# Kernel tuning notes

Hardware: AMD Instinct MI355X
Metric: run time of the kernel (lower is better)

Reference implementation:

```python
import jax, jax.numpy as jnp
import numpy as np

B, C1, C2, CF, H, W, NH = 1, 64, 256, 256, 64, 64, 8
HD = CF // NH
EPS = 1e-5


def setup_inputs() -> dict:
    key = jax.random.key(0)
    ks = jax.random.split(key, 12)
    s = 0.02
    return {
        "F_lidar": jax.random.normal(ks[0], (B, C1, H, W), jnp.float32),
        "F_cam": jax.random.normal(ks[1], (B, C2, H, W), jnp.float32),
        "Wq": jax.random.normal(ks[2], (CF, C1), jnp.float32) * s,
        "Wk": jax.random.normal(ks[3], (CF, C2), jnp.float32) * s,
        "Wv": jax.random.normal(ks[4], (CF, C2), jnp.float32) * s,
        "Wo": jax.random.normal(ks[5], (CF, CF), jnp.float32) * s,
        "Wres": jax.random.normal(ks[6], (CF, C1), jnp.float32) * s,
        "ln1_g": jnp.ones((CF,), jnp.float32),
        "ln1_b": jnp.zeros((CF,), jnp.float32),
        "ln2_g": jnp.ones((CF,), jnp.float32),
        "ln2_b": jnp.zeros((CF,), jnp.float32),
        "W1": jax.random.normal(ks[7], (4 * CF, CF), jnp.float32) * s,
        "b1": jnp.zeros((4 * CF,), jnp.float32),
        "W2": jax.random.normal(ks[8], (CF, 4 * CF), jnp.float32) * s,
        "b2": jnp.zeros((CF,), jnp.float32),
    }


def _ln(x, g, b):
    m = jnp.mean(x, axis=-1, keepdims=True)
    v = jnp.mean((x - m) ** 2, axis=-1, keepdims=True)
    return (x - m) * jax.lax.rsqrt(v + EPS) * g + b


def reference(F_lidar, F_cam, Wq, Wk, Wv, Wo, Wres, ln1_g, ln1_b, ln2_g, ln2_b, W1, b1, W2, b2):
    N = H * W
    # 1x1 convs == per-token linear projections on flattened tokens
    tok_l = F_lidar.reshape(B, C1, N).transpose(0, 2, 1)  # (B, N, C1)
    tok_c = F_cam.reshape(B, C2, N).transpose(0, 2, 1)    # (B, N, C2)
    Q = (tok_l @ Wq.T).reshape(B, N, NH, HD)
    K = (tok_c @ Wk.T).reshape(B, N, NH, HD)
    V = (tok_c @ Wv.T).reshape(B, N, NH, HD)
    scale = HD ** -0.5
    scores = jnp.einsum("bnhd,bmhd->bhnm", Q, K) * scale  # (B, NH, N, N)
    attn = jax.nn.softmax(scores, axis=-1)
    out = jnp.einsum("bhnm,bmhd->bnhd", attn, V).reshape(B, N, CF)
    out = out @ Wo.T                                      # out_proj (1x1 conv)
    res = tok_l @ Wres.T                                  # residual_proj
    x = _ln(res + out, ln1_g, ln1_b)
    # FFN (dropout is identity in eval)
    h = jax.nn.relu(x @ W1.T + b1)
    ffn = h @ W2.T + b2
    x = _ln(x + ffn, ln2_g, ln2_b)
    return x.transpose(0, 2, 1).reshape(B, CF, H, W)
```

## Files before the change

kernel.cpp:

```cpp
#include <hip/hip_runtime.h>
#include <math.h>

#define NTOK 4096
#define C1 64
#define C2 256
#define CF 256
#define NH 8
#define HD 32
#define CFF 1024
#define EPSF 1e-5f
#define SPLIT 4
#define KVBLK 128
#define QSCALE 0.25505654040876564f

using f32x4  = __attribute__((ext_vector_type(4))) float;
using bf16x8 = __attribute__((ext_vector_type(8))) short;
using u32x4  = __attribute__((ext_vector_type(4))) unsigned int;
typedef unsigned short ushort_t;

__device__ inline ushort_t f2bf(float x) {
    union { float f; unsigned int u; } v; v.f = x;
    unsigned int r = (v.u + 0x7FFFu + ((v.u >> 16) & 1u)) >> 16;
    return (ushort_t)r;
}
__device__ inline float bf2f(ushort_t u) {
    union { unsigned int i; float f; } v; v.i = ((unsigned int)u) << 16; return v.f;
}
__device__ inline unsigned int fbits(float x) {
    union { float f; unsigned int u; } v; v.f = x; return v.u;
}

__device__ inline float exp2_raw(float x) {
#if __has_builtin(__builtin_amdgcn_exp2f)
    return __builtin_amdgcn_exp2f(x);
#else
    float r;
    asm("v_exp_f32 %0, %1" : "=v"(r) : "v"(x));
    return r;
#endif
}

__global__ __launch_bounds__(256) void prep_kernel(
    const float* __restrict__ Wq, const float* __restrict__ Wk,
    const float* __restrict__ Wv, const float* __restrict__ Wo,
    const float* __restrict__ Wres, const float* __restrict__ W1,
    const float* __restrict__ W2, const float* __restrict__ F_lidar,
    const float* __restrict__ F_cam,
    ushort_t* oWq, ushort_t* oWk, ushort_t* oWv, ushort_t* oWo,
    ushort_t* oWres, ushort_t* oW1, ushort_t* oW2,
    ushort_t* __restrict__ Flt, ushort_t* __restrict__ Fct) {
    __shared__ float tls[32][33];
    int b = blockIdx.x;
    if (b < 736) {
        const float* src; ushort_t* dst; int base, lgK; bool tiled;
        if      (b < 16)  { src = Wq;   dst = oWq;   base = b;       lgK = 6;  tiled = false; }
        else if (b < 80)  { src = Wk;   dst = oWk;   base = b - 16;  lgK = 8;  tiled = false; }
        else if (b < 144) { src = Wv;   dst = oWv;   base = b - 80;  lgK = 8;  tiled = false; }
        else if (b < 208) { src = Wo;   dst = oWo;   base = b - 144; lgK = 8;  tiled = true; }
        else if (b < 224) { src = Wres; dst = oWres; base = b - 208; lgK = 6;  tiled = true; }
        else if (b < 480) { src = W1;   dst = oW1;   base = b - 224; lgK = 8;  tiled = true; }
        else              { src = W2;   dst = oW2;   base = b - 480; lgK = 10; tiled = true; }
        const int i = base * 1024 + threadIdx.x * 4;
        const float4 v = *(const float4*)(src + i);
        ushort4 pk;
        pk.x = f2bf(v.x); pk.y = f2bf(v.y); pk.z = f2bf(v.z); pk.w = f2bf(v.w);
        if (!tiled) {
            *(ushort4*)(dst + i) = pk;
        } else {
            const int c  = i >> lgK;
            const int kk = i & ((1 << lgK) - 1);
            const int tau = (c >> 8) * (1 << (lgK - 6)) + (kk >> 6);
            const int dst4 = tau * 16384 + (c & 255) * 64
                           + (((((kk >> 3) & 7)) ^ (c & 7)) << 3) + (kk & 7);
            *(ushort4*)(dst + dst4) = pk;
        }
        return;
    }
    b -= 736;
    const float* src; ushort_t* dst; int C, c0, n0;
    if (b < 256) { src = F_lidar; dst = Flt; C = C1; c0 = (b & 1) * 32; n0 = (b >> 1) * 32; }
    else { b -= 256; src = F_cam; dst = Fct; C = C2; c0 = (b & 7) * 32; n0 = (b >> 3) * 32; }
    const int tx = threadIdx.x & 31, ty = threadIdx.x >> 5;
#pragma unroll
    for (int i = 0; i < 32; i += 8) tls[ty + i][tx] = src[(size_t)(c0 + ty + i) * NTOK + n0 + tx];
    __syncthreads();
#pragma unroll
    for (int i = 0; i < 32; i += 8) dst[(size_t)(n0 + ty + i) * C + c0 + tx] = f2bf(tls[tx][ty + i]);
}

__global__ __launch_bounds__(256) void qkv_kernel(
    const ushort_t* __restrict__ Flt, const ushort_t* __restrict__ Fct,
    const ushort_t* __restrict__ Wqb, const ushort_t* __restrict__ Wkb,
    const ushort_t* __restrict__ Wvb,
    ushort_t* __restrict__ Qb, ushort_t* __restrict__ Kb, ushort_t* __restrict__ Vt) {
    const int z = blockIdx.z;
    const ushort_t* A = (z == 0) ? Flt : Fct;
    const ushort_t* W = (z == 0) ? Wqb : (z == 1) ? Wkb : Wvb;
    const int K = (z == 0) ? C1 : C2;

    const int tid = threadIdx.x;
    const int wid = tid >> 6, lane = tid & 63;
    const int g = lane >> 4, r = lane & 15;
    const int r0 = blockIdx.x * 128 + wid * 16;
    const int c0 = blockIdx.y * 64;

    f32x4 acc[2][4];
#pragma unroll
    for (int i = 0; i < 2; ++i)
#pragma unroll
        for (int t = 0; t < 4; ++t) acc[i][t] = (f32x4){0, 0, 0, 0};

    const ushort_t* ap0 = A + (size_t)(r0 + r) * K + (g << 3);
    const ushort_t* ap1 = ap0 + (size_t)64 * K;
    const ushort_t* wp = W + (size_t)(c0 + r) * K + (g << 3);
#pragma unroll 2
    for (int k0 = 0; k0 < K; k0 += 32) {
        const bf16x8 a0 = *(const bf16x8*)(ap0 + k0);
        const bf16x8 a1 = *(const bf16x8*)(ap1 + k0);
#pragma unroll
        for (int t = 0; t < 4; ++t) {
            const bf16x8 wf = *(const bf16x8*)(wp + (size_t)(t * 16) * K + k0);
            acc[0][t] = __builtin_amdgcn_mfma_f32_16x16x32_bf16(a0, wf, acc[0][t], 0, 0, 0);
            acc[1][t] = __builtin_amdgcn_mfma_f32_16x16x32_bf16(a1, wf, acc[1][t], 0, 0, 0);
        }
    }
    if (z == 0) {
#pragma unroll
        for (int i = 0; i < 2; ++i)
#pragma unroll
            for (int t = 0; t < 4; ++t) {
                const int col = c0 + 16 * t + r;
#pragma unroll
                for (int q = 0; q < 4; ++q)
                    Qb[(size_t)(r0 + i * 64 + 4 * g + q) * CF + col] = f2bf(acc[i][t][q] * QSCALE);
            }
    } else if (z == 1) {
#pragma unroll
        for (int i = 0; i < 2; ++i)
#pragma unroll
            for (int t = 0; t < 4; ++t) {
                const int col = c0 + 16 * t + r;
#pragma unroll
                for (int q = 0; q < 4; ++q) {
                    const int tok = r0 + i * 64 + 4 * g + q;
                    const int cs = (col & ~31) | ((((col >> 3) & 3) ^ ((tok >> 1) & 3)) << 3) | (col & 7);
                    Kb[(size_t)tok * CF + cs] = f2bf(acc[i][t][q]);
                }
            }
    } else {
#pragma unroll
        for (int i = 0; i < 2; ++i)
#pragma unroll
            for (int t = 0; t < 4; ++t) {
                const int dglob = c0 + 16 * t + r;
                const int hh = dglob >> 5, d = dglob & 31;
                const int tok0 = r0 + i * 64 + 4 * g;
                const int T = tok0 >> 7, tl = tok0 & 127;
                const int kc = tl >> 5, gp = (tl >> 2) & 3, jh = (tl >> 4) & 1;
                const int c = kc * 4 + gp;
                ushort4 pk;
                pk.x = f2bf(acc[i][t][0]); pk.y = f2bf(acc[i][t][1]);
                pk.z = f2bf(acc[i][t][2]); pk.w = f2bf(acc[i][t][3]);
                *(ushort4*)((char*)Vt + ((size_t)(hh * 32 + T) << 13)
                            + ((size_t)(c * 32 + (d ^ (c & 7))) << 4) + (jh << 3)) = pk;
            }
    }
}

__global__ __launch_bounds__(512, 4) void fattn_kernel(const ushort_t* __restrict__ Qb,
                                                       const ushort_t* __restrict__ Kb,
                                                       const ushort_t* __restrict__ Vt,
                                                       ushort_t* __restrict__ Opart,
                                                       float* __restrict__ Lst) {
    __shared__ ushort_t Ks[3][4096];
    __shared__ ushort_t Vs[2][4096];

    const int tid = threadIdx.x;
    const int wid = tid >> 6, lane = tid & 63;
    const int g = lane >> 4, r = lane & 15;
    const int bid = blockIdx.x;
    const int qb = bid & 15;
    const int sp = (bid >> 4) & (SPLIT - 1);
    const int h  = bid >> 6;
    const int n0 = qb * 256 + wid * 32;
    const int m_beg = sp * (NTOK / SPLIT);

    const bf16x8 qfA = *(const bf16x8*)(Qb + ((size_t)(n0 + r) << 8) + h * HD + (g << 3));
    const bf16x8 qfB = *(const bf16x8*)(Qb + ((size_t)(n0 + 16 + r) << 8) + h * HD + (g << 3));
    const bf16x8 onesf = {(short)0x3F80, (short)0x3F80, (short)0x3F80, (short)0x3F80,
                          (short)0x3F80, (short)0x3F80, (short)0x3F80, (short)0x3F80};

    const char* kb  = (const char*)Ks[0] + (r << 6) + ((g ^ ((r >> 1) & 3)) << 4);
    const char* vbg = (const char*)Vs[0] + (g << 9) + ((r & 8) << 4);
    const int slotbase = ((r & 7) ^ g) << 4;

    const int o = tid << 4;
    const char* ksrc = (const char*)Kb + (size_t)(m_beg + (o >> 6)) * 512 + (h << 6) + (o & 63);
    const char* vsrc = (const char*)Vt + ((size_t)(h * 32 + (m_beg >> 7)) << 13) + o;

    auto stageK = [&](int buf) {
        __builtin_amdgcn_global_load_lds(
            (const __attribute__((address_space(1))) unsigned int*)ksrc,
            (__attribute__((address_space(3))) unsigned int*)((char*)Ks[buf] + (wid << 10)), 16, 0, 0);
        ksrc += KVBLK * 512;
    };
    auto stageV = [&](int buf) {
        __builtin_amdgcn_global_load_lds(
            (const __attribute__((address_space(1))) unsigned int*)vsrc,
            (__attribute__((address_space(3))) unsigned int*)((char*)Vs[buf] + (wid << 10)), 16, 0, 0);
        vsrc += 8192;
    };

    f32x4 accA0 = {0, 0, 0, 0}, accA1 = {0, 0, 0, 0}, laccA = {0, 0, 0, 0};
    f32x4 accB0 = {0, 0, 0, 0}, accB1 = {0, 0, 0, 0}, laccB = {0, 0, 0, 0};

    stageK(0);
    stageV(0);
    stageK(1);
    asm volatile("s_waitcnt vmcnt(1)" ::: "memory");
    __builtin_amdgcn_s_barrier();

    constexpr int NT = (NTOK / SPLIT) / KVBLK;
#pragma unroll
    for (int tt = 0; tt < NT; ++tt) {
        if (tt + 1 < NT) stageV((tt + 1) & 1);
        if (tt + 2 < NT) stageK((tt + 2) % 3);
        const int kofs = (tt % 3) << 13;
        const int vofs = (tt & 1) << 13;

        f32x4 sA[8], sB[8];
#pragma unroll
        for (int t8 = 0; t8 < 8; ++t8) {
            const bf16x8 kf = *(const bf16x8*)(kb + kofs + (t8 << 10));
            sA[t8] = __builtin_amdgcn_mfma_f32_16x16x32_bf16(kf, qfA, (f32x4){0, 0, 0, 0}, 0, 0, 0);
            sB[t8] = __builtin_amdgcn_mfma_f32_16x16x32_bf16(kf, qfB, (f32x4){0, 0, 0, 0}, 0, 0, 0);
        }
        u32x4 pkvA[4], pkvB[4];
#pragma unroll
        for (int t8 = 0; t8 < 8; ++t8) {
            const float a0 = exp2_raw(sA[t8][0]);
            const float a1 = exp2_raw(sA[t8][1]);
            const float a2 = exp2_raw(sA[t8][2]);
            const float a3 = exp2_raw(sA[t8][3]);
            pkvA[t8 >> 1][(t8 & 1) * 2]     = __builtin_amdgcn_perm(fbits(a1), fbits(a0), 0x07060302u);
            pkvA[t8 >> 1][(t8 & 1) * 2 + 1] = __builtin_amdgcn_perm(fbits(a3), fbits(a2), 0x07060302u);
        }
#pragma unroll
        for (int t8 = 0; t8 < 8; ++t8) {
            const float b0 = exp2_raw(sB[t8][0]);
            const float b1 = exp2_raw(sB[t8][1]);
            const float b2 = exp2_raw(sB[t8][2]);
            const float b3 = exp2_raw(sB[t8][3]);
            pkvB[t8 >> 1][(t8 & 1) * 2]     = __builtin_amdgcn_perm(fbits(b1), fbits(b0), 0x07060302u);
            pkvB[t8 >> 1][(t8 & 1) * 2 + 1] = __builtin_amdgcn_perm(fbits(b3), fbits(b2), 0x07060302u);
        }
#pragma unroll
        for (int kc = 0; kc < 4; ++kc) {
            union { u32x4 u; bf16x8 b; } puA, puB;
            puA.u = pkvA[kc]; puB.u = pkvB[kc];
            const bf16x8 pfA = puA.b, pfB = puB.b;
            laccA = __builtin_amdgcn_mfma_f32_16x16x32_bf16(pfA, onesf, laccA, 0, 0, 0);
            laccB = __builtin_amdgcn_mfma_f32_16x16x32_bf16(pfB, onesf, laccB, 0, 0, 0);
            const char* va = vbg + vofs + (kc << 11) + (slotbase ^ ((kc & 1) << 6));
            const bf16x8 vf0 = *(const bf16x8*)(va);
            const bf16x8 vf1 = *(const bf16x8*)(va + 256);
            accA0 = __builtin_amdgcn_mfma_f32_16x16x32_bf16(pfA, vf0, accA0, 0, 0, 0);
            accB0 = __builtin_amdgcn_mfma_f32_16x16x32_bf16(pfB, vf0, accB0, 0, 0, 0);
            accA1 = __builtin_amdgcn_mfma_f32_16x16x32_bf16(pfA, vf1, accA1, 0, 0, 0);
            accB1 = __builtin_amdgcn_mfma_f32_16x16x32_bf16(pfB, vf1, accB1, 0, 0, 0);
        }
        if (tt + 2 < NT)      { asm volatile("s_waitcnt vmcnt(1)" ::: "memory"); }
        else                  { asm volatile("s_waitcnt vmcnt(0)" ::: "memory"); }
        __builtin_amdgcn_s_barrier();
    }
    const size_t baseA = (size_t)(sp * NH + h) * NTOK + n0;
    const size_t baseB = baseA + 16;
    if (r == 0) {
        *(f32x4*)(Lst + baseA + 4 * g) = laccA;
        *(f32x4*)(Lst + baseB + 4 * g) = laccB;
    }
#pragma unroll
    for (int q = 0; q < 4; ++q) {
        const size_t rowbA = (baseA + 4 * g + q) * HD;
        Opart[rowbA + r]      = f2bf(accA0[q]);
        Opart[rowbA + 16 + r] = f2bf(accA1[q]);
        const size_t rowbB = (baseB + 4 * g + q) * HD;
        Opart[rowbB + r]      = f2bf(accB0[q]);
        Opart[rowbB + 16 + r] = f2bf(accB1[q]);
    }
}

__global__ __launch_bounds__(512) void tail_kernel(
    const ushort_t* __restrict__ Opart, const float* __restrict__ Lst,
    const ushort_t* __restrict__ Wo,
    const ushort_t* __restrict__ Flt, const ushort_t* __restrict__ Wres,
    const float* __restrict__ g1, const float* __restrict__ bt1,
    const ushort_t* __restrict__ W1, const float* __restrict__ b1,
    const ushort_t* __restrict__ W2, const float* __restrict__ b2,
    const float* __restrict__ g2, const float* __restrict__ bt2,
    float* __restrict__ out) {
    __shared__ ushort_t Wb[3][16384];
    __shared__ ushort_t As[16][264];
    __shared__ ushort_t Xs[16][264];
    __shared__ ushort_t Hs[16][1032];
    __shared__ ushort_t Fs[16][72];
    __shared__ float Bias[2304];
    __shared__ float redS[8][16], redQ[8][16];
    const int tid = threadIdx.x;
    const int wid = tid >> 6, lane = tid & 63;
    const int g = lane >> 4, r = lane & 15;
    const int row0 = blockIdx.x * 16;
    const int cw = wid * 32;

    const int wl00 = (cw + r) * 128 + ((g ^ (r & 7)) << 4);
    const int wl01 = wl00 + 2048;
    const int wl10 = (cw + r) * 128 + (((4 + g) ^ (r & 7)) << 4);
    const int wl11 = wl10 + 2048;

    const int wslice = (wid << 12) + ((lane & 63) << 4);
    auto stageW = [&](const ushort_t* src, int buf) {
        const char* s = (const char*)src + wslice;
        char* d = (char*)&Wb[buf][0] + wslice;
#pragma unroll
        for (int j = 0; j < 4; ++j) {
            __builtin_amdgcn_global_load_lds(
                (const __attribute__((address_space(1))) unsigned int*)(s + j * 1024),
                (__attribute__((address_space(3))) unsigned int*)(d + j * 1024), 16, 0, 0);
        }
    };
    auto wsrc = [&](int s) -> const ushort_t* {
        if (s < 4)  return Wo + (size_t)s * 16384;
        if (s == 4) return Wres;
        if (s < 21) return W1 + (size_t)(s - 5) * 16384;
        return W2 + (size_t)(s - 21) * 16384;
    };

    {
        const int ri = tid >> 5;
        const int cc = (tid & 31) << 3;
        const int h  = cc >> 5, d0 = cc & 31;
        const int n  = row0 + ri;
        float L = 0.f;
#pragma unroll
        for (int s = 0; s < SPLIT; ++s) L += Lst[(size_t)(s * NH + h) * NTOK + n];
        const float invL = 1.f / L;
        float o[8] = {0.f, 0.f, 0.f, 0.f, 0.f, 0.f, 0.f, 0.f};
#pragma unroll
        for (int s = 0; s < SPLIT; ++s) {
            const ushort_t* p = Opart + ((size_t)(s * NH + h) * NTOK + n) * HD + d0;
            const ushort4 a = *(const ushort4*)p;
            const ushort4 b = *(const ushort4*)(p + 4);
            o[0] += bf2f(a.x); o[1] += bf2f(a.y); o[2] += bf2f(a.z); o[3] += bf2f(a.w);
            o[4] += bf2f(b.x); o[5] += bf2f(b.y); o[6] += bf2f(b.z); o[7] += bf2f(b.w);
        }
        ushort4 m0, m1;
        m0.x = f2bf(o[0] * invL); m0.y = f2bf(o[1] * invL);
        m0.z = f2bf(o[2] * invL); m0.w = f2bf(o[3] * invL);
        m1.x = f2bf(o[4] * invL); m1.y = f2bf(o[5] * invL);
        m1.z = f2bf(o[6] * invL); m1.w = f2bf(o[7] * invL);
        *(ushort4*)&As[ri][cc]     = m0;
        *(ushort4*)&As[ri][cc + 4] = m1;
        *(ushort2*)&Fs[ri][(tid & 31) * 2] =
            *(const ushort2*)(Flt + (size_t)(row0 + ri) * C1 + (tid & 31) * 2);
#pragma unroll
        for (int i5 = 0; i5 < 5; ++i5) {
            const int i = i5 * 512 + tid;
            if (i < 2304) {
                float v;
                if      (i < 256)  v = g1[i];
                else if (i < 512)  v = bt1[i - 256];
                else if (i < 768)  v = b2[i - 512];
                else if (i < 1024) v = g2[i - 768];
                else if (i < 1280) v = bt2[i - 1024];
                else               v = b1[i - 1280];
                Bias[i] = v;
            }
        }
    }
    __syncthreads();

    stageW(wsrc(0), 0);
    stageW(wsrc(1), 1);

    f32x4 accB[2] = {{0, 0, 0, 0}, {0, 0, 0, 0}};
#pragma unroll
    for (int t = 0; t < 5; ++t) {
        stageW(wsrc(t + 2), (t + 2) % 3);
        asm volatile("s_waitcnt vmcnt(8)" ::: "memory");
        const char* wb = (const char*)&Wb[t % 3][0];
        const bf16x8 w00 = *(const bf16x8*)(wb + wl00);
        const bf16x8 w01 = *(const bf16x8*)(wb + wl01);
        const bf16x8 w10 = *(const bf16x8*)(wb + wl10);
        const bf16x8 w11 = *(const bf16x8*)(wb + wl11);
        bf16x8 af0, af1;
        if (t < 4) {
            af0 = *(const bf16x8*)&As[r][t * 64 + (g << 3)];
            af1 = *(const bf16x8*)&As[r][t * 64 + 32 + (g << 3)];
        } else {
            af0 = *(const bf16x8*)&Fs[r][(g << 3)];
            af1 = *(const bf16x8*)&Fs[r][32 + (g << 3)];
        }
        accB[0] = __builtin_amdgcn_mfma_f32_16x16x32_bf16(af0, w00, accB[0], 0, 0, 0);
        accB[1] = __builtin_amdgcn_mfma_f32_16x16x32_bf16(af0, w01, accB[1], 0, 0, 0);
        accB[0] = __builtin_amdgcn_mfma_f32_16x16x32_bf16(af1, w10, accB[0], 0, 0, 0);
        accB[1] = __builtin_amdgcn_mfma_f32_16x16x32_bf16(af1, w11, accB[1], 0, 0, 0);
    }
    f32x4 xv[2];
    {
        f32x4 sv, qv;
#pragma unroll
        for (int q = 0; q < 4; ++q) {
            float s = accB[0][q] + accB[1][q];
            float sq = fmaf(accB[0][q], accB[0][q], accB[1][q] * accB[1][q]);
            s += __shfl_xor(s, 1); s += __shfl_xor(s, 2); s += __shfl_xor(s, 4); s += __shfl_xor(s, 8);
            sq += __shfl_xor(sq, 1); sq += __shfl_xor(sq, 2); sq += __shfl_xor(sq, 4); sq += __shfl_xor(sq, 8);
            sv[q] = s; qv[q] = sq;
        }
        if (r == 0) { *(f32x4*)&redS[wid][4 * g] = sv; *(f32x4*)&redQ[wid][4 * g] = qv; }
        __syncthreads();
        f32x4 S = {0, 0, 0, 0}, SQ = {0, 0, 0, 0};
#pragma unroll
        for (int w = 0; w < 8; ++w) {
            S  += *(const f32x4*)&redS[w][4 * g];
            SQ += *(const f32x4*)&redQ[w][4 * g];
        }
        f32x4 mn4, rs4;
#pragma unroll
        for (int q = 0; q < 4; ++q) {
            mn4[q] = S[q] * (1.f / CF);
            rs4[q] = rsqrtf(fmaxf(SQ[q] * (1.f / CF) - mn4[q] * mn4[q], 0.f) + EPSF);
        }
#pragma unroll
        for (int t = 0; t < 2; ++t) {
            const int col = cw + 16 * t + r;
            const float gam = Bias[col], bet = Bias[256 + col];
#pragma unroll
            for (int q = 0; q < 4; ++q) {
                xv[t][q] = (accB[t][q] - mn4[q]) * rs4[q] * gam + bet;
                Xs[4 * g + q][col] = f2bf(xv[t][q]);
            }
        }
    }
    __syncthreads();

    {
        f32x4 acc1[8];
#pragma unroll
        for (int t = 0; t < 8; ++t) acc1[t] = (f32x4){0, 0, 0, 0};
#pragma unroll
        for (int t = 5; t < 21; ++t) {
            stageW(wsrc(t + 2), (t + 2) % 3);
            asm volatile("s_waitcnt vmcnt(8)" ::: "memory");
            const int tc = t - 5;
            const char* wb = (const char*)&Wb[t % 3][0];
            const bf16x8 w00 = *(const bf16x8*)(wb + wl00);
            const bf16x8 w01 = *(const bf16x8*)(wb + wl01);
            const bf16x8 w10 = *(const bf16x8*)(wb + wl10);
            const bf16x8 w11 = *(const bf16x8*)(wb + wl11);
            const bf16x8 af0 = *(const bf16x8*)&Xs[r][(tc & 3) * 64 + (g << 3)];
            const bf16x8 af1 = *(const bf16x8*)&Xs[r][(tc & 3) * 64 + 32 + (g << 3)];
            const int idx = (tc >> 2) * 2;
            acc1[idx]     = __builtin_amdgcn_mfma_f32_16x16x32_bf16(w00, af0, acc1[idx], 0, 0, 0);
            acc1[idx + 1] = __builtin_amdgcn_mfma_f32_16x16x32_bf16(w01, af0, acc1[idx + 1], 0, 0, 0);
            acc1[idx]     = __builtin_amdgcn_mfma_f32_16x16x32_bf16(w10, af1, acc1[idx], 0, 0, 0);
            acc1[idx + 1] = __builtin_amdgcn_mfma_f32_16x16x32_bf16(w11, af1, acc1[idx + 1], 0, 0, 0);
        }
#pragma unroll
        for (int idx = 0; idx < 8; ++idx) {
            const int colb = (idx >> 1) * 256 + cw + 16 * (idx & 1) + 4 * g;
            const f32x4 bv = *(const f32x4*)&Bias[1280 + colb];
            ushort4 hw;
            hw.x = f2bf(fmaxf(acc1[idx][0] + bv[0], 0.f));
            hw.y = f2bf(fmaxf(acc1[idx][1] + bv[1], 0.f));
            hw.z = f2bf(fmaxf(acc1[idx][2] + bv[2], 0.f));
            hw.w = f2bf(fmaxf(acc1[idx][3] + bv[3], 0.f));
            *(ushort4*)&Hs[r][colb] = hw;
        }
    }
    __syncthreads();

    f32x4 accD[2] = {{0, 0, 0, 0}, {0, 0, 0, 0}};
#pragma unroll
    for (int t = 21; t < 37; ++t) {
        if (t + 2 < 37) {
            stageW(wsrc(t + 2), (t + 2) % 3);
            asm volatile("s_waitcnt vmcnt(8)" ::: "memory");
        } else if (t + 1 < 37) {
            asm volatile("s_waitcnt vmcnt(4)" ::: "memory");
        } else {
            asm volatile("s_waitcnt vmcnt(0)" ::: "memory");
        }
        const int tc = t - 21;
        const char* wb = (const char*)&Wb[t % 3][0];
        const bf16x8 w00 = *(const bf16x8*)(wb + wl00);
        const bf16x8 w01 = *(const bf16x8*)(wb + wl01);
        const bf16x8 w10 = *(const bf16x8*)(wb + wl10);
        const bf16x8 w11 = *(const bf16x8*)(wb + wl11);
        const bf16x8 af0 = *(const bf16x8*)&Hs[r][tc * 64 + (g << 3)];
        const bf16x8 af1 = *(const bf16x8*)&Hs[r][tc * 64 + 32 + (g << 3)];
        accD[0] = __builtin_amdgcn_mfma_f32_16x16x32_bf16(af0, w00, accD[0], 0, 0, 0);
        accD[1] = __builtin_amdgcn_mfma_f32_16x16x32_bf16(af0, w01, accD[1], 0, 0, 0);
        accD[0] = __builtin_amdgcn_mfma_f32_16x16x32_bf16(af1, w10, accD[0], 0, 0, 0);
        accD[1] = __builtin_amdgcn_mfma_f32_16x16x32_bf16(af1, w11, accD[1], 0, 0, 0);
    }
    {
#pragma unroll
        for (int t = 0; t < 2; ++t) {
            const float bb = Bias[512 + cw + 16 * t + r];
#pragma unroll
            for (int q = 0; q < 4; ++q) accD[t][q] += bb + xv[t][q];
        }
        f32x4 sv, qv;
#pragma unroll
        for (int q = 0; q < 4; ++q) {
            float s = accD[0][q] + accD[1][q];
            float sq = fmaf(accD[0][q], accD[0][q], accD[1][q] * accD[1][q]);
            s += __shfl_xor(s, 1); s += __shfl_xor(s, 2); s += __shfl_xor(s, 4); s += __shfl_xor(s, 8);
            sq += __shfl_xor(sq, 1); sq += __shfl_xor(sq, 2); sq += __shfl_xor(sq, 4); sq += __shfl_xor(sq, 8);
            sv[q] = s; qv[q] = sq;
        }
        __syncthreads();
        if (r == 0) { *(f32x4*)&redS[wid][4 * g] = sv; *(f32x4*)&redQ[wid][4 * g] = qv; }
        __syncthreads();
        f32x4 S = {0, 0, 0, 0}, SQ = {0, 0, 0, 0};
#pragma unroll
        for (int w = 0; w < 8; ++w) {
            S  += *(const f32x4*)&redS[w][4 * g];
            SQ += *(const f32x4*)&redQ[w][4 * g];
        }
        f32x4 mn4, rs4;
#pragma unroll
        for (int q = 0; q < 4; ++q) {
            mn4[q] = S[q] * (1.f / CF);
            rs4[q] = rsqrtf(fmaxf(SQ[q] * (1.f / CF) - mn4[q] * mn4[q], 0.f) + EPSF);
        }
#pragma unroll
        for (int t = 0; t < 2; ++t) {
            const int col = cw + 16 * t + r;
            const float gam = Bias[768 + col], bet = Bias[1024 + col];
            f32x4 ov;
#pragma unroll
            for (int q = 0; q < 4; ++q)
                ov[q] = (accD[t][q] - mn4[q]) * rs4[q] * gam + bet;
            *(f32x4*)(out + (size_t)col * NTOK + row0 + 4 * g) = ov;
        }
    }
}

extern "C" void kernel_launch(void* const* d_in, const int* in_sizes, int n_in,
                              void* d_out, int out_size, void* d_ws, size_t ws_size,
                              hipStream_t stream) {
    const float* F_lidar = (const float*)d_in[0];
    const float* F_cam   = (const float*)d_in[1];
    const float* Wq      = (const float*)d_in[2];
    const float* Wk      = (const float*)d_in[3];
    const float* Wv      = (const float*)d_in[4];
    const float* Wo      = (const float*)d_in[5];
    const float* Wres    = (const float*)d_in[6];
    const float* ln1_g   = (const float*)d_in[7];
    const float* ln1_b   = (const float*)d_in[8];
    const float* ln2_g   = (const float*)d_in[9];
    const float* ln2_b   = (const float*)d_in[10];
    const float* W1      = (const float*)d_in[11];
    const float* b1      = (const float*)d_in[12];
    const float* W2      = (const float*)d_in[13];
    const float* b2      = (const float*)d_in[14];
    float* out = (float*)d_out;
    char* ws = (char*)d_ws;

    const size_t KB = 1024, MB = 1024 * 1024;
    ushort_t* Wq_b   = (ushort_t*)(ws + 0);
    ushort_t* Wk_b   = (ushort_t*)(ws + 32 * KB);
    ushort_t* Wv_b   = (ushort_t*)(ws + 160 * KB);
    ushort_t* Wo_b   = (ushort_t*)(ws + 288 * KB);
    ushort_t* Wres_b = (ushort_t*)(ws + 416 * KB);
    ushort_t* W1_b   = (ushort_t*)(ws + 448 * KB);
    ushort_t* W2_b   = (ushort_t*)(ws + 960 * KB);
    ushort_t* Flt    = (ushort_t*)(ws + 1536 * KB);
    ushort_t* Fct    = (ushort_t*)(ws + 2 * MB);
    ushort_t* Qb     = (ushort_t*)(ws + 4 * MB);
    ushort_t* Kb     = (ushort_t*)(ws + 6 * MB);
    ushort_t* Vt     = (ushort_t*)(ws + 8 * MB);
    ushort_t* Opart  = (ushort_t*)(ws + 12 * MB);
    float*    Lst    = (float*)(ws + 20 * MB);

    prep_kernel<<<2016, 256, 0, stream>>>(Wq, Wk, Wv, Wo, Wres, W1, W2, F_lidar, F_cam,
                                          Wq_b, Wk_b, Wv_b, Wo_b, Wres_b, W1_b, W2_b, Flt, Fct);
    qkv_kernel<<<dim3(NTOK / 128, CF / 64, 3), 256, 0, stream>>>(Flt, Fct, Wq_b, Wk_b, Wv_b, Qb, Kb, Vt);
    fattn_kernel<<<NH * SPLIT * (NTOK / 256), 512, 0, stream>>>(Qb, Kb, Vt, Opart, Lst);
    tail_kernel<<<NTOK / 16, 512, 0, stream>>>(Opart, Lst, Wo_b, Flt, Wres_b, ln1_g, ln1_b,
                                               W1_b, b1, W2_b, b2, ln2_g, ln2_b, out);
}
```

Measured before the change: 63.62 us.

## Double per-wave query rows in flash attention to reuse K/V tiles

Each wave in the attention kernel now processes 64 query rows instead of 32 (four 16-row fragments), and each block covers 512 queries, so the grid is halved. K fragments are loaded into registers once and reused across four QK MFMAs, and each V fragment feeds four PV MFMAs. This halves K/V staging traffic and LDS reads per query. The cost is much higher register pressure (launch bounds lowered from 4 to 2 blocks per CU) and only 256 blocks, which may underfill the GPU and reduce latency hiding.

```diff
diff --git a/kernel.cpp b/kernel.cpp
--- a/kernel.cpp
+++ b/kernel.cpp
@@ -167,7 +167,7 @@
     }
 }
 
-__global__ __launch_bounds__(512, 4) void fattn_kernel(const ushort_t* __restrict__ Qb,
+__global__ __launch_bounds__(512, 2) void fattn_kernel(const ushort_t* __restrict__ Qb,
                                                        const ushort_t* __restrict__ Kb,
                                                        const ushort_t* __restrict__ Vt,
                                                        ushort_t* __restrict__ Opart,
@@ -179,14 +179,16 @@
     const int wid = tid >> 6, lane = tid & 63;
     const int g = lane >> 4, r = lane & 15;
     const int bid = blockIdx.x;
-    const int qb = bid & 15;
-    const int sp = (bid >> 4) & (SPLIT - 1);
-    const int h  = bid >> 6;
-    const int n0 = qb * 256 + wid * 32;
+    const int qb = bid & 7;
+    const int sp = (bid >> 3) & (SPLIT - 1);
+    const int h  = bid >> 5;
+    const int n0 = qb * 512 + wid * 64;
     const int m_beg = sp * (NTOK / SPLIT);
 
-    const bf16x8 qfA = *(const bf16x8*)(Qb + ((size_t)(n0 + r) << 8) + h * HD + (g << 3));
-    const bf16x8 qfB = *(const bf16x8*)(Qb + ((size_t)(n0 + 16 + r) << 8) + h * HD + (g << 3));
+    bf16x8 qf[4];
+#pragma unroll
+    for (int i = 0; i < 4; ++i)
+        qf[i] = *(const bf16x8*)(Qb + ((size_t)(n0 + 16 * i + r) << 8) + h * HD + (g << 3));
     const bf16x8 onesf = {(short)0x3F80, (short)0x3F80, (short)0x3F80, (short)0x3F80,
                           (short)0x3F80, (short)0x3F80, (short)0x3F80, (short)0x3F80};
 
@@ -211,8 +213,13 @@
         vsrc += 8192;
     };
 
-    f32x4 accA0 = {0, 0, 0, 0}, accA1 = {0, 0, 0, 0}, laccA = {0, 0, 0, 0};
-    f32x4 accB0 = {0, 0, 0, 0}, accB1 = {0, 0, 0, 0}, laccB = {0, 0, 0, 0};
+    f32x4 acc0[4], acc1[4], lacc[4];
+#pragma unroll
+    for (int i = 0; i < 4; ++i) {
+        acc0[i] = (f32x4){0, 0, 0, 0};
+        acc1[i] = (f32x4){0, 0, 0, 0};
+        lacc[i] = (f32x4){0, 0, 0, 0};
+    }
 
     stageK(0);
     stageV(0);
@@ -228,65 +235,86 @@
         const int kofs = (tt % 3) << 13;
         const int vofs = (tt & 1) << 13;
 
-        f32x4 sA[8], sB[8];
-#pragma unroll
-        for (int t8 = 0; t8 < 8; ++t8) {
-            const bf16x8 kf = *(const bf16x8*)(kb + kofs + (t8 << 10));
-            sA[t8] = __builtin_amdgcn_mfma_f32_16x16x32_bf16(kf, qfA, (f32x4){0, 0, 0, 0}, 0, 0, 0);
-            sB[t8] = __builtin_amdgcn_mfma_f32_16x16x32_bf16(kf, qfB, (f32x4){0, 0, 0, 0}, 0, 0, 0);
-        }
-        u32x4 pkvA[4], pkvB[4];
-#pragma unroll
-        for (int t8 = 0; t8 < 8; ++t8) {
-            const float a0 = exp2_raw(sA[t8][0]);
-            const float a1 = exp2_raw(sA[t8][1]);
-            const float a2 = exp2_raw(sA[t8][2]);
-            const float a3 = exp2_raw(sA[t8][3]);
-            pkvA[t8 >> 1][(t8 & 1) * 2]     = __builtin_amdgcn_perm(fbits(a1), fbits(a0), 0x07060302u);
-            pkvA[t8 >> 1][(t8 & 1) * 2 + 1] = __builtin_amdgcn_perm(fbits(a3), fbits(a2), 0x07060302u);
-        }
-#pragma unroll
-        for (int t8 = 0; t8 < 8; ++t8) {
-            const float b0 = exp2_raw(sB[t8][0]);
-            const float b1 = exp2_raw(sB[t8][1]);
-            const float b2 = exp2_raw(sB[t8][2]);
-            const float b3 = exp2_raw(sB[t8][3]);
-            pkvB[t8 >> 1][(t8 & 1) * 2]     = __builtin_amdgcn_perm(fbits(b1), fbits(b0), 0x07060302u);
-            pkvB[t8 >> 1][(t8 & 1) * 2 + 1] = __builtin_amdgcn_perm(fbits(b3), fbits(b2), 0x07060302u);
+        bf16x8 kfr[8];
+#pragma unroll
+        for (int t8 = 0; t8 < 8; ++t8)
+            kfr[t8] = *(const bf16x8*)(kb + kofs + (t8 << 10));
+
+        u32x4 pkv[4][4];
+        {
+            f32x4 sA[8], sB[8];
+#pragma unroll
+            for (int t8 = 0; t8 < 8; ++t8) {
+                sA[t8] = __builtin_amdgcn_mfma_f32_16x16x32_bf16(kfr[t8], qf[0], (f32x4){0, 0, 0, 0}, 0, 0, 0);
+                sB[t8] = __builtin_amdgcn_mfma_f32_16x16x32_bf16(kfr[t8], qf[1], (f32x4){0, 0, 0, 0}, 0, 0, 0);
+            }
+#pragma unroll
+            for (int t8 = 0; t8 < 8; ++t8) {
+                const float a0 = exp2_raw(sA[t8][0]);
+                const float a1 = exp2_raw(sA[t8][1]);
+                const float a2 = exp2_raw(sA[t8][2]);
+                const float a3 = exp2_raw(sA[t8][3]);
+                pkv[0][t8 >> 1][(t8 & 1) * 2]     = __builtin_amdgcn_perm(fbits(a1), fbits(a0), 0x07060302u);
+                pkv[0][t8 >> 1][(t8 & 1) * 2 + 1] = __builtin_amdgcn_perm(fbits(a3), fbits(a2), 0x07060302u);
+                const float b0 = exp2_raw(sB[t8][0]);
+                const float b1 = exp2_raw(sB[t8][1]);
+                const float b2 = exp2_raw(sB[t8][2]);
+                const float b3 = exp2_raw(sB[t8][3]);
+                pkv[1][t8 >> 1][(t8 & 1) * 2]     = __builtin_amdgcn_perm(fbits(b1), fbits(b0), 0x07060302u);
+                pkv[1][t8 >> 1][(t8 & 1) * 2 + 1] = __builtin_amdgcn_perm(fbits(b3), fbits(b2), 0x07060302u);
+            }
+        }
+        {
+            f32x4 sA[8], sB[8];
+#pragma unroll
+            for (int t8 = 0; t8 < 8; ++t8) {
+                sA[t8] = __builtin_amdgcn_mfma_f32_16x16x32_bf16(kfr[t8], qf[2], (f32x4){0, 0, 0, 0}, 0, 0, 0);
+                sB[t8] = __builtin_amdgcn_mfma_f32_16x16x32_bf16(kfr[t8], qf[3], (f32x4){0, 0, 0, 0}, 0, 0, 0);
+            }
+#pragma unroll
+            for (int t8 = 0; t8 < 8; ++t8) {
+                const float a0 = exp2_raw(sA[t8][0]);
+                const float a1 = exp2_raw(sA[t8][1]);
+                const float a2 = exp2_raw(sA[t8][2]);
+                const float a3 = exp2_raw(sA[t8][3]);
+                pkv[2][t8 >> 1][(t8 & 1) * 2]     = __builtin_amdgcn_perm(fbits(a1), fbits(a0), 0x07060302u);
+                pkv[2][t8 >> 1][(t8 & 1) * 2 + 1] = __builtin_amdgcn_perm(fbits(a3), fbits(a2), 0x07060302u);
+                const float b0 = exp2_raw(sB[t8][0]);
+                const float b1 = exp2_raw(sB[t8][1]);
+                const float b2 = exp2_raw(sB[t8][2]);
+                const float b3 = exp2_raw(sB[t8][3]);
+                pkv[3][t8 >> 1][(t8 & 1) * 2]     = __builtin_amdgcn_perm(fbits(b1), fbits(b0), 0x07060302u);
+                pkv[3][t8 >> 1][(t8 & 1) * 2 + 1] = __builtin_amdgcn_perm(fbits(b3), fbits(b2), 0x07060302u);
+            }
         }
 #pragma unroll
         for (int kc = 0; kc < 4; ++kc) {
-            union { u32x4 u; bf16x8 b; } puA, puB;
-            puA.u = pkvA[kc]; puB.u = pkvB[kc];
-            const bf16x8 pfA = puA.b, pfB = puB.b;
-            laccA = __builtin_amdgcn_mfma_f32_16x16x32_bf16(pfA, onesf, laccA, 0, 0, 0);
-            laccB = __builtin_amdgcn_mfma_f32_16x16x32_bf16(pfB, onesf, laccB, 0, 0, 0);
             const char* va = vbg + vofs + (kc << 11) + (slotbase ^ ((kc & 1) << 6));
             const bf16x8 vf0 = *(const bf16x8*)(va);
             const bf16x8 vf1 = *(const bf16x8*)(va + 256);
-            accA0 = __builtin_amdgcn_mfma_f32_16x16x32_bf16(pfA, vf0, accA0, 0, 0, 0);
-            accB0 = __builtin_amdgcn_mfma_f32_16x16x32_bf16(pfB, vf0, accB0, 0, 0, 0);
-            accA1 = __builtin_amdgcn_mfma_f32_16x16x32_bf16(pfA, vf1, accA1, 0, 0, 0);
-            accB1 = __builtin_amdgcn_mfma_f32_16x16x32_bf16(pfB, vf1, accB1, 0, 0, 0);
-        }
-        if (tt + 2 < NT)      { asm volatile("s_waitcnt vmcnt(1)" ::: "memory"); }
-        else                  { asm volatile("s_waitcnt vmcnt(0)" ::: "memory"); }
+#pragma unroll
+            for (int i = 0; i < 4; ++i) {
+                union { u32x4 u; bf16x8 b; } pu; pu.u = pkv[i][kc];
+                const bf16x8 pf = pu.b;
+                lacc[i] = __builtin_amdgcn_mfma_f32_16x16x32_bf16(pf, onesf, lacc[i], 0, 0, 0);
+                acc0[i] = __builtin_amdgcn_mfma_f32_16x16x32_bf16(pf, vf0, acc0[i], 0, 0, 0);
+                acc1[i] = __builtin_amdgcn_mfma_f32_16x16x32_bf16(pf, vf1, acc1[i], 0, 0, 0);
+            }
+        }
+        if (tt + 2 < NT) { asm volatile("s_waitcnt vmcnt(1)" ::: "memory"); }
+        else             { asm volatile("s_waitcnt vmcnt(0)" ::: "memory"); }
         __builtin_amdgcn_s_barrier();
     }
-    const size_t baseA = (size_t)(sp * NH + h) * NTOK + n0;
-    const size_t baseB = baseA + 16;
-    if (r == 0) {
-        *(f32x4*)(Lst + baseA + 4 * g) = laccA;
-        *(f32x4*)(Lst + baseB + 4 * g) = laccB;
-    }
-#pragma unroll
-    for (int q = 0; q < 4; ++q) {
-        const size_t rowbA = (baseA + 4 * g + q) * HD;
-        Opart[rowbA + r]      = f2bf(accA0[q]);
-        Opart[rowbA + 16 + r] = f2bf(accA1[q]);
-        const size_t rowbB = (baseB + 4 * g + q) * HD;
-        Opart[rowbB + r]      = f2bf(accB0[q]);
-        Opart[rowbB + 16 + r] = f2bf(accB1[q]);
+#pragma unroll
+    for (int i = 0; i < 4; ++i) {
+        const size_t base = (size_t)(sp * NH + h) * NTOK + n0 + 16 * i;
+        if (r == 0) *(f32x4*)(Lst + base + 4 * g) = lacc[i];
+#pragma unroll
+        for (int q = 0; q < 4; ++q) {
+            const size_t rowb = (base + 4 * g + q) * HD;
+            Opart[rowb + r]      = f2bf(acc0[i][q]);
+            Opart[rowb + 16 + r] = f2bf(acc1[i][q]);
+        }
     }
 }
 
@@ -587,7 +615,7 @@
     prep_kernel<<<2016, 256, 0, stream>>>(Wq, Wk, Wv, Wo, Wres, W1, W2, F_lidar, F_cam,
                                           Wq_b, Wk_b, Wv_b, Wo_b, Wres_b, W1_b, W2_b, Flt, Fct);
     qkv_kernel<<<dim3(NTOK / 128, CF / 64, 3), 256, 0, stream>>>(Flt, Fct, Wq_b, Wk_b, Wv_b, Qb, Kb, Vt);
-    fattn_kernel<<<NH * SPLIT * (NTOK / 256), 512, 0, stream>>>(Qb, Kb, Vt, Opart, Lst);
+    fattn_kernel<<<NH * SPLIT * (NTOK / 512), 512, 0, stream>>>(Qb, Kb, Vt, Opart, Lst);
     tail_kernel<<<NTOK / 16, 512, 0, stream>>>(Opart, Lst, Wo_b, Flt, Wres_b, ln1_g, ln1_b,
                                                W1_b, b1, W2_b, b2, ln2_g, ln2_b, out);
 }
```

Measured after the change: 65.91 us. 3.6% more time.
